# Kernel tuning notes

Hardware: AMD Instinct MI355X
Metric: run time of the kernel (lower is better)

## Reference

```python
import jax, jax.numpy as jnp
import numpy as np

B, S = 64, 512
VOCAB, D, H, NH = 50000, 256, 256, 4
MAX_DUR = 12.0
SCALE_RATE = 1.0


def setup_inputs() -> dict:
    key = jax.random.key(0)
    ks = jax.random.split(key, 12)
    s = 1.0 / np.sqrt(H)
    inp = {
        "src": jax.random.randint(ks[0], (B, S), 0, VOCAB),
        "input_len": jax.random.randint(ks[1], (B,), 1, S + 1),
        "fix_src": jax.random.uniform(ks[2], (B, S), jnp.float32) * MAX_DUR,
        "emb_table": jax.random.normal(ks[3], (VOCAB, D), jnp.float32) * 0.02,
        "Wi": jax.random.uniform(ks[4], (H, D), jnp.float32, -s, s),
        "bi": jax.random.uniform(ks[5], (H,), jnp.float32, -s, s),
        "Wh": jax.random.uniform(ks[6], (H, NH * H), jnp.float32, -s, s),
        "bh": jax.random.uniform(ks[7], (H,), jnp.float32, -s, s),
        "fc1_W": jax.random.uniform(ks[8], (D, NH * H), jnp.float32, -s, s),
        "fc1_b": jax.random.uniform(ks[9], (D,), jnp.float32, -s, s),
        "fc2_W": jax.random.uniform(ks[10], (2, D), jnp.float32, -s, s),
        "fc2_b": jax.random.uniform(ks[11], (2,), jnp.float32, -s, s),
    }
    return inp


def _forward(src, input_len, fix_src, emb_table, Wi, bi, Wh, bh, fc1_W, fc1_b, fc2_W, fc2_b):
    emb = emb_table[src]                      # [B, S, D]
    offsets = jnp.arange(NH, dtype=emb.dtype) * (MAX_DUR / NH)  # [NH]
    h0 = jnp.zeros((NH, B, H), emb.dtype)

    def step(h, xd):
        x, d = xd                             # x [B,D], d [B]
        hcat = jnp.swapaxes(h, 0, 1).reshape(B, NH * H)
        cand = jnp.tanh(x @ Wi.T + bi + hcat @ Wh.T + bh)        # [B,H]
        g = jax.nn.sigmoid(d[:, None] * SCALE_RATE - offsets)    # [B,NH]
        gt = g.T[:, :, None]                                     # [NH,B,1]
        h_new = gt * cand[None, :, :] + (1.0 - gt) * h           # [NH,B,H]
        out = jnp.swapaxes(h_new, 0, 1).reshape(B, NH * H)
        return h_new, out

    xs = (jnp.swapaxes(emb, 0, 1), fix_src.T)  # [S,B,D], [S,B]
    _, outs = jax.lax.scan(step, h0, xs)       # [S, B, NH*H]
    outs = jnp.swapaxes(outs, 0, 1)            # [B, S, NH*H]
    sel = outs[jnp.arange(B), input_len - 1]   # gather at last valid step, [B, NH*H]
    hid = jnp.tanh(sel @ fc1_W.T + fc1_b)      # [B, D]
    return hid @ fc2_W.T + fc2_b               # [B, 2]


def reference(src, input_len, fix_src, emb_table, Wi, bi, Wh, bh, fc1_W, fc1_b, fc2_W, fc2_b):
    return _forward(src, input_len, fix_src, emb_table, Wi, bi, Wh, bh, fc1_W, fc1_b, fc2_W, fc2_b)
```

## Files before the change

### kernel.cpp

```cpp
#include <hip/hip_runtime.h>
#include <stdint.h>

constexpr int BB = 64;
constexpr int SS = 512;
constexpr int DD = 256;
constexpr int HH = 256;
constexpr int NHH = 4;
constexpr int KK = 1024;

constexpr int TT = 512;

typedef _Float16 f16;
typedef _Float16 f16x2 __attribute__((ext_vector_type(2)));

__device__ inline float dot2p(uint32_t a, uint32_t b, float c) {
  f16x2 av = __builtin_bit_cast(f16x2, a);
  f16x2 bv = __builtin_bit_cast(f16x2, b);
#if defined(__has_builtin)
#if __has_builtin(__builtin_amdgcn_fdot2)
  return __builtin_amdgcn_fdot2(av, bv, c, false);
#else
  return c + (float)av.x * (float)bv.x + (float)av.y * (float)bv.y;
#endif
#else
  return c + (float)av.x * (float)bv.x + (float)av.y * (float)bv.y;
#endif
}

__device__ inline float dot8(uint4 w, uint4 a, float c) {
  c = dot2p(w.x, a.x, c);
  c = dot2p(w.y, a.y, c);
  c = dot2p(w.z, a.z, c);
  c = dot2p(w.w, a.w, c);
  return c;
}

__device__ inline uint32_t pack2(float a, float b) {
  f16x2 v;
  v.x = (f16)a;
  v.y = (f16)b;
  return __builtin_bit_cast(uint32_t, v);
}

__device__ inline float fast_tanh(float x) {
  x = fminf(fmaxf(x, -15.f), 15.f);
  float e = __expf(2.f * x);
  return 1.f - 2.f / (e + 1.f);
}

__global__ void k_pack_wq(const float* __restrict__ Wh, uint4* __restrict__ Wq) {
  int gid = blockIdx.x * blockDim.x + threadIdx.x;
  int p = gid >> 13;
  int m = (gid >> 9) & 15;
  int t = gid & 511;
  int out = t & 255, ch2 = t >> 8;
  int n = out >> 6, o_loc = out & 63;
  const float* s = Wh + (64 * p + o_loc) * KK + 256 * n + 128 * ch2 + 8 * m;
  uint4 w;
  w.x = pack2(s[0], s[1]);
  w.y = pack2(s[2], s[3]);
  w.z = pack2(s[4], s[5]);
  w.w = pack2(s[6], s[7]);
  Wq[gid] = w;
}

__global__ void k_transpose8(const float* __restrict__ src, float* __restrict__ dst,
                             int C, int total) {
  int gid = blockIdx.x * blockDim.x + threadIdx.x;
  if (gid >= total) return;
  int r = gid & 255, c = gid >> 8;
  dst[gid] = src[r * C + c];
}

__global__ __launch_bounds__(256) void k_precompute_u(
    const int* __restrict__ src, const float* __restrict__ emb,
    const float* __restrict__ WiT, const float* __restrict__ bi,
    const float* __restrict__ bh, const int* __restrict__ input_len,
    f16* __restrict__ U) {
  const int row0 = blockIdx.x * 32;
  const int b = row0 >> 9;
  if ((row0 & 511) >= input_len[b]) return;
  __shared__ float xs[32 * 256];
  __shared__ int srcs[32];
  const int tid = threadIdx.x;
  if (tid < 32) srcs[tid] = src[row0 + tid];
  __syncthreads();
  for (int i = tid; i < 32 * 256; i += 256) {
    int r = i >> 8, d = i & 255;
    xs[i] = emb[srcs[r] * DD + d];
  }
  __syncthreads();
  const int o = tid;
  float acc[32];
#pragma unroll
  for (int r = 0; r < 32; ++r) acc[r] = 0.f;
  for (int d0 = 0; d0 < 256; d0 += 8) {
    float w[8];
#pragma unroll
    for (int j = 0; j < 8; ++j) w[j] = WiT[(d0 + j) * 256 + o];
#pragma unroll
    for (int r = 0; r < 32; ++r) {
      const float4* xp = (const float4*)(xs + r * 256 + d0);
      float4 x0 = xp[0], x1 = xp[1];
      acc[r] += x0.x * w[0] + x0.y * w[1] + x0.z * w[2] + x0.w * w[3] +
                x1.x * w[4] + x1.y * w[5] + x1.z * w[6] + x1.w * w[7];
    }
  }
  float bias = bi[o] + bh[o];
#pragma unroll
  for (int r = 0; r < 32; ++r)
    U[(size_t)(row0 + r) * HH + o] = (f16)(acc[r] + bias);
}

__global__ void __attribute__((amdgpu_flat_work_group_size(512, 512),
                               amdgpu_waves_per_eu(4, 4)))
k_recurrence(
    const uint4* __restrict__ Wq, const f16* __restrict__ U,
    const float* __restrict__ fix_src, const int* __restrict__ input_len,
    const float* __restrict__ fc1T, const float* __restrict__ fc1_b,
    const float* __restrict__ fc2_W, const float* __restrict__ fc2_b,
    float* __restrict__ out, uint32_t* __restrict__ Cex,
    float* __restrict__ FPg, int* __restrict__ Flg) {
  __shared__ __align__(16) char arena[61440];
  f16* cbuf = (f16*)arena;
  uint4* cvec = (uint4*)arena;
  float* partials = (float*)(arena + 512);
  float* hbuf = (float*)(arena + 2560);

  const int idx = blockIdx.x;
  const int b = idx & 63;
  const int p = idx >> 6;
  const int t = threadIdx.x;
  const int out_i = t & 255, ch2 = t >> 8;
  const int n = out_i >> 6, o_loc = out_i & 63;

  uint4 w[16];
  const uint4* wp = Wq + (p * 16) * TT + t;
#pragma unroll
  for (int m = 0; m < 16; ++m) w[m] = wp[m * TT];
#pragma unroll
  for (int m = 0; m < 16; ++m)
    asm volatile("" : "+v"(w[m].x), "+v"(w[m].y), "+v"(w[m].z), "+v"(w[m].w));

  float v0 = 0.f, v1 = 0.f, v2 = 0.f, v3 = 0.f;
  float h = 0.f;

  const int len = input_len[b];
  const f16* Ub = U + (size_t)b * SS * HH;
  const float* fsb = fix_src + b * SS;

  if (t < 64) {
    float c0 = fast_tanh((float)Ub[64 * p + t]);
    f16 chv = (f16)c0;
    cbuf[64 * p + t] = chv;
    uint32_t dwp =
        ((uint32_t)__builtin_bit_cast(unsigned short, chv) << 16) | 1u;
    __hip_atomic_store(&Cex[b * 256 + p * 64 + t], dwp, __ATOMIC_RELAXED,
                       __HIP_MEMORY_SCOPE_AGENT);
  }

#pragma unroll 1
  for (int s = 0; s < len; ++s) {
#pragma unroll
    for (int m = 0; m < 16; ++m)
      asm volatile("" : "+v"(w[m].x), "+v"(w[m].y), "+v"(w[m].z), "+v"(w[m].w));

    const int par = s & 1;
    const uint32_t tag = (uint32_t)((s + 1) & 0xffff);
    const float dval = fsb[s];
    float g = 0.f, gq1 = 0.f, gq2 = 0.f, gq3 = 0.f, ufn = 0.f;

    if (t < 64) {
      int sn = (s + 1 < len) ? (s + 1) : s;
      ufn = (float)Ub[(size_t)sn * HH + 64 * p + t];
      g   = 1.f / (1.f + __expf(0.f - dval));
      gq1 = 1.f / (1.f + __expf(3.f - dval));
      gq2 = 1.f / (1.f + __expf(6.f - dval));
      gq3 = 1.f / (1.f + __expf(9.f - dval));
    } else if (t < 256) {
      g = 1.f / (1.f + __expf((float)(3 * n) - dval));
      int wv = t >> 6;
      int lane = t & 63;
      int q = (p + wv) & 3;
      uint32_t* addr = &Cex[((par * 64 + b) * 4 + q) * 64 + lane];
      uint32_t dw;
      do {
        dw = __hip_atomic_load(addr, __ATOMIC_RELAXED,
                               __HIP_MEMORY_SCOPE_AGENT);
      } while ((dw & 0xffffu) != tag);
      cbuf[64 * q + lane] =
          __builtin_bit_cast(f16, (unsigned short)(dw >> 16));
    }
    __syncthreads();

    float acc = 0.f;
    const uint4* ap = cvec + ch2 * 16;
#pragma unroll
    for (int m = 0; m < 16; ++m) acc = dot8(w[m], ap[m], acc);
    partials[t] = acc;

    if (t < 256) {
      float cown = (float)cbuf[64 * p + o_loc];
      h = g * cown + (1.f - g) * h;
    }
    __syncthreads();

    if (t < 64) {
      float w0 = partials[t]       + partials[256 + t];
      float w1 = partials[64 + t]  + partials[320 + t];
      float w2 = partials[128 + t] + partials[384 + t];
      float w3 = partials[192 + t] + partials[448 + t];
      v0 = g   * w0 + (1.f - g)   * v0;
      v1 = gq1 * w1 + (1.f - gq1) * v1;
      v2 = gq2 * w2 + (1.f - gq2) * v2;
      v3 = gq3 * w3 + (1.f - gq3) * v3;
      float c = fast_tanh(ufn + (v0 + v1 + v2 + v3));
      f16 chv = (f16)c;
      uint32_t dwp =
          ((uint32_t)__builtin_bit_cast(unsigned short, chv) << 16) |
          (uint32_t)((s + 2) & 0xffff);
      __hip_atomic_store(
          &Cex[(((s + 1) & 1) * 64 + b) * 256 + p * 64 + t], dwp,
          __ATOMIC_RELAXED, __HIP_MEMORY_SCOPE_AGENT);
      cbuf[64 * p + t] = chv;
    }
  }

  if (t < 256) hbuf[out_i] = h;
  __syncthreads();
  {
    float acc = 0.f;
#pragma unroll 4
    for (int r = 0; r < 128; ++r) {
      int k_loc = ch2 * 128 + r;
      int n2 = k_loc >> 6, il = k_loc & 63;
      int kg = n2 * 256 + 64 * p + il;
      acc += hbuf[k_loc] * fc1T[(size_t)kg * 256 + out_i];
    }
    partials[t] = acc;
  }
  __syncthreads();
  if (t < 256) FPg[(b * 4 + p) * 256 + out_i] =
      partials[out_i] + partials[256 + out_i];
  __syncthreads();
  if (t == 0)
    __hip_atomic_store(&Flg[b * 4 + p], 0x5A5A5A5A, __ATOMIC_RELEASE,
                       __HIP_MEMORY_SCOPE_AGENT);
  if (p != 0) return;
  if (t < 4 && t > 0) {
    while (__hip_atomic_load(&Flg[b * 4 + t], __ATOMIC_ACQUIRE,
                             __HIP_MEMORY_SCOPE_AGENT) != 0x5A5A5A5A) {
    }
  }
  __syncthreads();
  if (t < 256) {
    float pre = fc1_b[t];
#pragma unroll
    for (int q = 0; q < 4; ++q)
      pre += __hip_atomic_load(&FPg[(b * 4 + q) * 256 + t], __ATOMIC_RELAXED,
                               __HIP_MEMORY_SCOPE_AGENT);
    hbuf[t] = fast_tanh(pre);
  }
  __syncthreads();
  if (t < 64) {
    float p0 = 0.f, p1 = 0.f;
    for (int oi = t; oi < 256; oi += 64) {
      float hh = hbuf[oi];
      p0 += hh * fc2_W[oi];
      p1 += hh * fc2_W[256 + oi];
    }
#pragma unroll
    for (int off = 32; off; off >>= 1) {
      p0 += __shfl_down(p0, off);
      p1 += __shfl_down(p1, off);
    }
    if (t == 0) {
      out[b * 2 + 0] = p0 + fc2_b[0];
      out[b * 2 + 1] = p1 + fc2_b[1];
    }
  }
}

extern "C" void kernel_launch(void* const* d_in, const int* in_sizes, int n_in,
                              void* d_out, int out_size, void* d_ws, size_t ws_size,
                              hipStream_t stream) {
  const int* src = (const int*)d_in[0];
  const int* input_len = (const int*)d_in[1];
  const float* fix_src = (const float*)d_in[2];
  const float* emb = (const float*)d_in[3];
  const float* Wi = (const float*)d_in[4];
  const float* bi = (const float*)d_in[5];
  const float* Wh = (const float*)d_in[6];
  const float* bh = (const float*)d_in[7];
  const float* fc1_W = (const float*)d_in[8];
  const float* fc1_b = (const float*)d_in[9];
  const float* fc2_W = (const float*)d_in[10];
  const float* fc2_b = (const float*)d_in[11];
  float* out = (float*)d_out;

  char* ws = (char*)d_ws;
  uint4* Wq = (uint4*)(ws);
  float* WiT = (float*)(ws + (512ull << 10));
  float* fc1T = (float*)(ws + (768ull << 10));
  f16* U = (f16*)(ws + (1792ull << 10));
  uint32_t* Cex = (uint32_t*)(ws + (18176ull << 10));
  float* FPg = (float*)(ws + (18304ull << 10));
  int* Flg = (int*)(ws + (18560ull << 10));
  const size_t needed = (18561ull << 10);
  if (ws_size < needed) return;

  k_pack_wq<<<128, 256, 0, stream>>>(Wh, Wq);
  k_transpose8<<<(65536 + 255) / 256, 256, 0, stream>>>(Wi, WiT, 256, 65536);
  k_transpose8<<<(262144 + 255) / 256, 256, 0, stream>>>(fc1_W, fc1T, 1024, 262144);
  k_precompute_u<<<BB * SS / 32, 256, 0, stream>>>(src, emb, WiT, bi, bh,
                                                   input_len, U);
  k_recurrence<<<BB * 4, TT, 0, stream>>>(Wq, U, fix_src, input_len, fc1T,
                                          fc1_b, fc2_W, fc2_b, out, Cex, FPg,
                                          Flg);
}
```

Before: 760.9 us.

## Stage recurrent weights in swizzled LDS instead of holding them in registers

The packed fp16 recurrent weights move from 64 per-thread VGPRs into a 128 KB dynamic LDS buffer. The pack kernel now writes them in an XOR-swizzled per-thread row order so that the LDS reads inside the recurrence avoid bank conflicts. The waves-per-EU hint is dropped, and the kernel raises its max dynamic shared memory attribute once so the large allocation is allowed. This frees register pressure, but in exchange every serial time step adds 16 wide LDS reads to the latency-critical loop.

New measurement: 834.5 us. +9.7%, slower.

```diff
diff --git a/kernel.cpp b/kernel.cpp
--- a/kernel.cpp
+++ b/kernel.cpp
@@ -9,6 +9,7 @@
 constexpr int KK = 1024;
 
 constexpr int TT = 512;
+constexpr int RECUR_LDS = 134656;
 
 typedef _Float16 f16;
 typedef _Float16 f16x2 __attribute__((ext_vector_type(2)));
@@ -51,8 +52,9 @@
 __global__ void k_pack_wq(const float* __restrict__ Wh, uint4* __restrict__ Wq) {
   int gid = blockIdx.x * blockDim.x + threadIdx.x;
   int p = gid >> 13;
-  int m = (gid >> 9) & 15;
-  int t = gid & 511;
+  int t = (gid >> 4) & 511;
+  int j = gid & 15;
+  int m = j ^ (t & 15);
   int out = t & 255, ch2 = t >> 8;
   int n = out >> 6, o_loc = out & 63;
   const float* s = Wh + (64 * p + o_loc) * KK + 256 * n + 128 * ch2 + 8 * m;
@@ -112,8 +114,7 @@
     U[(size_t)(row0 + r) * HH + o] = (f16)(acc[r] + bias);
 }
 
-__global__ void __attribute__((amdgpu_flat_work_group_size(512, 512),
-                               amdgpu_waves_per_eu(4, 4)))
+__global__ void __attribute__((amdgpu_flat_work_group_size(512, 512)))
 k_recurrence(
     const uint4* __restrict__ Wq, const f16* __restrict__ U,
     const float* __restrict__ fix_src, const int* __restrict__ input_len,
@@ -121,11 +122,12 @@
     const float* __restrict__ fc2_W, const float* __restrict__ fc2_b,
     float* __restrict__ out, uint32_t* __restrict__ Cex,
     float* __restrict__ FPg, int* __restrict__ Flg) {
-  __shared__ __align__(16) char arena[61440];
-  f16* cbuf = (f16*)arena;
-  uint4* cvec = (uint4*)arena;
-  float* partials = (float*)(arena + 512);
-  float* hbuf = (float*)(arena + 2560);
+  extern __shared__ __align__(16) char arena[];
+  uint4* wl = (uint4*)arena;
+  f16* cbuf = (f16*)(arena + 131072);
+  uint4* cvec = (uint4*)(arena + 131072);
+  float* partials = (float*)(arena + 131584);
+  float* hbuf = (float*)(arena + 133632);
 
   const int idx = blockIdx.x;
   const int b = idx & 63;
@@ -134,13 +136,11 @@
   const int out_i = t & 255, ch2 = t >> 8;
   const int n = out_i >> 6, o_loc = out_i & 63;
 
-  uint4 w[16];
-  const uint4* wp = Wq + (p * 16) * TT + t;
-#pragma unroll
-  for (int m = 0; m < 16; ++m) w[m] = wp[m * TT];
-#pragma unroll
-  for (int m = 0; m < 16; ++m)
-    asm volatile("" : "+v"(w[m].x), "+v"(w[m].y), "+v"(w[m].z), "+v"(w[m].w));
+  {
+    const uint4* wsrc = Wq + p * 8192;
+#pragma unroll
+    for (int k2 = 0; k2 < 16; ++k2) wl[t + 512 * k2] = wsrc[t + 512 * k2];
+  }
 
   float v0 = 0.f, v1 = 0.f, v2 = 0.f, v3 = 0.f;
   float h = 0.f;
@@ -159,12 +159,11 @@
                        __HIP_MEMORY_SCOPE_AGENT);
   }
 
+  const int tsw = t & 15;
+  const uint4* wrow = wl + t * 16;
+
 #pragma unroll 1
   for (int s = 0; s < len; ++s) {
-#pragma unroll
-    for (int m = 0; m < 16; ++m)
-      asm volatile("" : "+v"(w[m].x), "+v"(w[m].y), "+v"(w[m].z), "+v"(w[m].w));
-
     const int par = s & 1;
     const uint32_t tag = (uint32_t)((s + 1) & 0xffff);
     const float dval = fsb[s];
@@ -196,7 +195,7 @@
     float acc = 0.f;
     const uint4* ap = cvec + ch2 * 16;
 #pragma unroll
-    for (int m = 0; m < 16; ++m) acc = dot8(w[m], ap[m], acc);
+    for (int m = 0; m < 16; ++m) acc = dot8(wrow[m ^ tsw], ap[m], acc);
     partials[t] = acc;
 
     if (t < 256) {
@@ -309,12 +308,19 @@
   const size_t needed = (18561ull << 10);
   if (ws_size < needed) return;
 
+  static bool attr_set = false;
+  if (!attr_set) {
+    hipFuncSetAttribute((const void*)k_recurrence,
+                        hipFuncAttributeMaxDynamicSharedMemorySize, RECUR_LDS);
+    attr_set = true;
+  }
+
   k_pack_wq<<<128, 256, 0, stream>>>(Wh, Wq);
   k_transpose8<<<(65536 + 255) / 256, 256, 0, stream>>>(Wi, WiT, 256, 65536);
   k_transpose8<<<(262144 + 255) / 256, 256, 0, stream>>>(fc1_W, fc1T, 1024, 262144);
   k_precompute_u<<<BB * SS / 32, 256, 0, stream>>>(src, emb, WiT, bi, bh,
                                                    input_len, U);
-  k_recurrence<<<BB * 4, TT, 0, stream>>>(Wq, U, fix_src, input_len, fc1T,
-                                          fc1_b, fc2_W, fc2_b, out, Cex, FPg,
-                                          Flg);
-}
+  k_recurrence<<<BB * 4, TT, RECUR_LDS, stream>>>(Wq, U, fix_src, input_len,
+                                                  fc1T, fc1_b, fc2_W, fc2_b,
+                                                  out, Cex, FPg, Flg);
+}
```
